# Kernel tuning notes

Hardware: AMD Instinct MI355X
Metric: run time of the kernel (lower is better)

## Reference

```python
import jax, jax.numpy as jnp
import numpy as np

# ---- problem constants (match init_kwargs / input_specs) ----
N = 10000        # atoms
E = 160000       # edges
G = 16           # graphs in batch
Z = 10           # num_elements
K = 64           # channels (count of 0e in hidden_irreps)
NB = 8           # num_bessel
SH = 9           # (max_ell+1)^2, max_ell=2
HID = 16         # MLP_irreps 16x0e
R_MAX = 5.0
AVG_NEI = 16.0
P = 5            # num_polynomial_cutoff
L_SLICES = ((0, 1, 0), (1, 4, 1), (4, 9, 2))  # (start, end, l) per irrep block


def _sph(u):
    # real spherical harmonics, 'component' normalization, lmax=2 -> 9 comps
    x, y, z = u[:, 0], u[:, 1], u[:, 2]
    s3, s15, s5 = 3.0 ** 0.5, 15.0 ** 0.5, 5.0 ** 0.5
    one = jnp.ones_like(x)
    return jnp.stack([one,
                      s3 * x, s3 * y, s3 * z,
                      s15 * x * y, s15 * y * z,
                      0.5 * s5 * (3.0 * z * z - 1.0),
                      s15 * x * z, 0.5 * s15 * (x * x - y * y)], axis=-1)


def _radial(r):
    # Bessel basis * polynomial cutoff (p=5)
    n = jnp.arange(1, NB + 1, dtype=r.dtype)
    bess = (2.0 / R_MAX) ** 0.5 * jnp.sin(n[None, :] * jnp.pi * r[:, None] / R_MAX) / r[:, None]
    xx = r / R_MAX
    f = (1.0 - 0.5 * (P + 1) * (P + 2) * xx ** P + P * (P + 2) * xx ** (P + 1)
         - 0.5 * P * (P + 1) * xx ** (P + 2)) * (xx < 1.0)
    return bess * f[:, None]


def _total_energy(positions, node_attrs, shifts, atomic_energies, W_embed, W_up,
                  R1, R2, R3, R4, W_out, W_sc, theta, W_mix, w_read0, Wr1, Wr2,
                  edge_index, batch):
    sender, receiver = edge_index[0], edge_index[1]
    vec = positions[receiver] - positions[sender] + shifts          # [E,3]
    r = jnp.sqrt(jnp.sum(vec * vec, axis=-1) + 1e-9)                # [E]
    u = vec / r[:, None]
    sh = _sph(u)                                                     # [E,9]
    edge_feats = _radial(r)                                          # [E,NB]

    node_e0 = node_attrs @ atomic_energies                           # [N]
    energies = jax.ops.segment_sum(node_e0, batch, num_segments=G)   # [G]

    feats = node_attrs @ W_embed                                     # [N,K] scalar feats
    for i in range(2):
        h = feats @ W_up[i]                                          # [N,K]
        xw = jax.nn.silu(edge_feats @ R1[i])
        xw = jax.nn.silu(xw @ R2[i])
        xw = jax.nn.silu(xw @ R3[i])
        rw = xw @ R4[i]                                              # [E,K] TP weights
        # channel-wise tensor product message + scatter to receiver
        m = rw[:, :, None] * h[sender][:, :, None] * sh[:, None, :]  # [E,K,9]
        A = jax.ops.segment_sum(m, receiver, num_segments=N) / AVG_NEI  # [N,K,9]
        A = jnp.concatenate([jnp.einsum('nkc,kj->njc', A[:, :, s:e], W_out[i, l])
                             for (s, e, l) in L_SLICES], axis=-1)    # per-l linear
        sc = jnp.einsum('nk,nz,zkj->nj', feats, node_attrs, W_sc[i])  # residual (0e)
        # symmetric-contraction product block (correlation=3), element-dependent
        a0 = A[:, :, 0]
        w = jnp.einsum('nz,pzk->pnk', node_attrs, theta[i])           # [3,N,K]
        B = (w[0] + w[1] * a0 + w[2] * a0 * a0)[:, :, None] * A      # [N,K,9]
        B = jnp.einsum('nkc,kj->njc', B, W_mix[i])
        B = B.at[:, :, 0].add(sc)
        feats = B[:, :, 0]                                            # invariant part
        if i == 0:
            node_e = feats @ w_read0                                  # linear readout
        else:
            node_e = jax.nn.silu(feats @ Wr1) @ Wr2                   # nonlinear readout
        energies = energies + jax.ops.segment_sum(node_e, batch, num_segments=G)
    return energies                                                   # [G]


def setup_inputs() -> dict:
    key = jax.random.key(0)
    ks = jax.random.split(key, 24)
    positions = jax.random.normal(ks[0], (N, 3), jnp.float32) * 1.5
    elems = jax.random.randint(ks[1], (N,), 0, Z)
    node_attrs = jax.nn.one_hot(elems, Z, dtype=jnp.float32)
    edge_index = jax.random.randint(ks[2], (2, E), 0, N)
    batch = jnp.sort(jax.random.randint(ks[3], (N,), 0, G))
    shifts = jnp.zeros((E, 3), jnp.float32)
    rn = lambda k, sh, s: jax.random.normal(k, sh, jnp.float32) * s
    return {
        'positions': positions, 'node_attrs': node_attrs, 'shifts': shifts,
        'atomic_energies': rn(ks[4], (Z,), 1.0),
        'W_embed': rn(ks[5], (Z, K), Z ** -0.5),
        'W_up': rn(ks[6], (2, K, K), K ** -0.5),
        'R1': rn(ks[7], (2, NB, 64), NB ** -0.5),
        'R2': rn(ks[8], (2, 64, 64), 64 ** -0.5),
        'R3': rn(ks[9], (2, 64, 64), 64 ** -0.5),
        'R4': rn(ks[10], (2, 64, K), 64 ** -0.5),
        'W_out': rn(ks[11], (2, 3, K, K), K ** -0.5),
        'W_sc': rn(ks[12], (2, Z, K, K), (Z * K) ** -0.5),
        'theta': rn(ks[13], (2, 3, Z, K), 0.1),
        'W_mix': rn(ks[14], (2, K, K), K ** -0.5),
        'w_read0': rn(ks[15], (K,), K ** -0.5),
        'Wr1': rn(ks[16], (K, HID), K ** -0.5),
        'Wr2': rn(ks[17], (HID,), HID ** -0.5),
        'edge_index': edge_index, 'batch': batch,
    }


def reference(positions, node_attrs, shifts, atomic_energies, W_embed, W_up,
              R1, R2, R3, R4, W_out, W_sc, theta, W_mix, w_read0, Wr1, Wr2,
              edge_index, batch):
    def energy(pos):
        return _total_energy(pos, node_attrs, shifts, atomic_energies, W_embed, W_up,
                             R1, R2, R3, R4, W_out, W_sc, theta, W_mix,
                             w_read0, Wr1, Wr2, edge_index, batch)
    total_energy, vjp_fn = jax.vjp(energy, positions)
    (g_pos,) = vjp_fn(jnp.ones((G,), positions.dtype))
    forces = -g_pos
    return total_energy, forces
```

## Files before the change

kernel.cpp:

```cpp
#include <hip/hip_runtime.h>
#include <math.h>

#define N_NODES 10000
#define N_EDGES 160000
#define G_SEG 16
#define ZDIM 10
#define KDIM 64
#define NBESS 8
#define HIDR 16
#define RMAXF 5.0f
#define AVG_NEI_F 16.0f
#define TBINS 256

__device__ __forceinline__ float siluf(float x){ float s = 1.0f/(1.0f+expf(-x)); return x*s; }
__device__ __forceinline__ float dsiluf(float x){ float s = 1.0f/(1.0f+expf(-x)); return s*(1.0f + x*(1.0f-s)); }

__device__ __forceinline__ float waveReduce(float v){
  for (int off = 32; off > 0; off >>= 1) v += __shfl_down(v, off);
  return v;
}

__device__ __forceinline__ void r_decode(float r, int& b, float& fr, float& wm){
  wm = (r >= 0.f) ? 1.f : 0.f;
  float tp = fmaxf(r, 0.f) * (TBINS / RMAXF);
  b = (int)tp; if (b > TBINS-1) b = TBINS-1;
  fr = tp - (float)b;
}

#define GATHER_NODE(NODE, PTR, PACK, IDXEXPR, LOADH, OUT) { \
  int beg_ = PTR[NODE]; int deg_ = PTR[(NODE)+1] - beg_; \
  float a0_=0.f,a1_=0.f,a2_=0.f,a3_=0.f; \
  for (int base_=0; base_<deg_; base_+=64){ \
    int m_ = min(64, deg_-base_); \
    float r_l = -1.f; int ix_l = 0; \
    if (lane < m_){ int4 pk = PACK[beg_+base_+lane]; r_l = __int_as_float(pk.x); ix_l = IDXEXPR; } \
    int mr_ = (m_ + 7) & ~7; \
    for (int i_=0; i_<mr_; i_+=8){ \
      float r0_=__shfl(r_l,i_),   r1_=__shfl(r_l,i_+1), r2_=__shfl(r_l,i_+2), r3_=__shfl(r_l,i_+3); \
      float r4_=__shfl(r_l,i_+4), r5_=__shfl(r_l,i_+5), r6_=__shfl(r_l,i_+6), r7_=__shfl(r_l,i_+7); \
      int s0_=__shfl(ix_l,i_),   s1_=__shfl(ix_l,i_+1), s2_=__shfl(ix_l,i_+2), s3_=__shfl(ix_l,i_+3); \
      int s4_=__shfl(ix_l,i_+4), s5_=__shfl(ix_l,i_+5), s6_=__shfl(ix_l,i_+6), s7_=__shfl(ix_l,i_+7); \
      int b0_,b1_,b2_,b3_,b4_,b5_,b6_,b7_; \
      float f0_,f1_,f2_,f3_,f4_,f5_,f6_,f7_, w0_,w1_,w2_,w3_,w4_,w5_,w6_,w7_; \
      r_decode(r0_,b0_,f0_,w0_); r_decode(r1_,b1_,f1_,w1_); r_decode(r2_,b2_,f2_,w2_); r_decode(r3_,b3_,f3_,w3_); \
      r_decode(r4_,b4_,f4_,w4_); r_decode(r5_,b5_,f5_,w5_); r_decode(r6_,b6_,f6_,w6_); r_decode(r7_,b7_,f7_,w7_); \
      float2 F0_=Ft2[b0_*KDIM+lane]; float h0_=LOADH(s0_); \
      float2 F1_=Ft2[b1_*KDIM+lane]; float h1_=LOADH(s1_); \
      float2 F2_=Ft2[b2_*KDIM+lane]; float h2_=LOADH(s2_); \
      float2 F3_=Ft2[b3_*KDIM+lane]; float h3_=LOADH(s3_); \
      float2 F4_=Ft2[b4_*KDIM+lane]; float h4_=LOADH(s4_); \
      float2 F5_=Ft2[b5_*KDIM+lane]; float h5_=LOADH(s5_); \
      float2 F6_=Ft2[b6_*KDIM+lane]; float h6_=LOADH(s6_); \
      float2 F7_=Ft2[b7_*KDIM+lane]; float h7_=LOADH(s7_); \
      a0_ += w0_*(F0_.x + f0_*(F0_.y-F0_.x))*h0_; a1_ += w1_*(F1_.x + f1_*(F1_.y-F1_.x))*h1_; \
      a2_ += w2_*(F2_.x + f2_*(F2_.y-F2_.x))*h2_; a3_ += w3_*(F3_.x + f3_*(F3_.y-F3_.x))*h3_; \
      a0_ += w4_*(F4_.x + f4_*(F4_.y-F4_.x))*h4_; a1_ += w5_*(F5_.x + f5_*(F5_.y-F5_.x))*h5_; \
      a2_ += w6_*(F6_.x + f6_*(F6_.y-F6_.x))*h6_; a3_ += w7_*(F7_.x + f7_*(F7_.y-F7_.x))*h7_; \
    } } \
  OUT = ((a0_+a1_)+(a2_+a3_)); }

#define COOPMV(INV, W, OUTV) { \
  lds_in[w][lane] = INV; \
  __syncthreads(); \
  { float p0_=0.f,p1_=0.f,p2_=0.f,p3__=0.f; \
    const float* Wb_ = (W) + (w*16)*KDIM + lane; \
    _Pragma("unroll") \
    for (int kk_=0; kk_<16; kk_++){ \
      float wrow_ = Wb_[kk_*KDIM]; \
      int k_ = w*16 + kk_; \
      p0_  += lds_in[0][k_]*wrow_; \
      p1_  += lds_in[1][k_]*wrow_; \
      p2_  += lds_in[2][k_]*wrow_; \
      p3__ += lds_in[3][k_]*wrow_; \
    } \
    lds_part[w][0][lane]=p0_; lds_part[w][1][lane]=p1_; \
    lds_part[w][2][lane]=p2_; lds_part[w][3][lane]=p3__; } \
  __syncthreads(); \
  OUTV = ((lds_part[0][w][lane]+lds_part[1][w][lane]) + \
          (lds_part[2][w][lane]+lds_part[3][w][lane])); }

#define MV4R(V, W, OUT) { \
  float x0_=0.f,x1_=0.f,x2_=0.f,x3_=0.f; \
  for (int k_=0;k_<KDIM;k_+=4){ \
    x0_ += __shfl(V,k_)  *W[k_*KDIM+lane]; \
    x1_ += __shfl(V,k_+1)*W[(k_+1)*KDIM+lane]; \
    x2_ += __shfl(V,k_+2)*W[(k_+2)*KDIM+lane]; \
    x3_ += __shfl(V,k_+3)*W[(k_+3)*KDIM+lane]; \
  } OUT = (x0_+x1_)+(x2_+x3_); }

#define LOADH_PLAIN(S) rows[(S)*KDIM + lane]
#define LOADH_G2(S)    gAr2c[(S)*KDIM + lane].x

__global__ __launch_bounds__(256) void k_setup(
    const float* We, const float* Wup, const float* Wsc,
    const float* Wout, const float* Wmix,
    const float* Wr1,
    const float* attrs, const float* aE,
    float* M0, float* Msc0,
    float* WoT0, float* WoT1, float* WmixT0, float* WupT1,
    float* P1, float* Qtab,
    int* z_buf, float* e_node){
  int blk = blockIdx.x, tid = threadIdx.x;
  const float* Wmix1 = Wmix + KDIM*KDIM;
  const float* Wsc1  = Wsc + ZDIM*KDIM*KDIM;
  if (blk < 5){
    int idx = blk*256 + tid;
    if (idx < 1280){
      int which = idx >= 640;
      int t = which ? idx - 640 : idx;
      int z = t >> 6, j = t & 63;
      float acc = 0.f;
      if (!which){
        #pragma unroll 8
        for (int k = 0; k < KDIM; k++) acc += We[z*KDIM + k] * Wup[k*KDIM + j];
        M0[z*KDIM + j] = acc;
      } else {
        #pragma unroll 8
        for (int k = 0; k < KDIM; k++) acc += We[z*KDIM + k] * Wsc[(z*KDIM + k)*KDIM + j];
        Msc0[z*KDIM + j] = acc;
      }
    }
  } else if (blk < 69){
    int t = (blk-5)*256 + tid;
    int arr = t >> 12;
    int rem = t & 4095;
    int j = rem >> 6, k = rem & 63;
    float v; float* dst;
    switch(arr){
      case 0: v = Wout[k*KDIM + j];                 dst = WoT0;   break;
      case 1: v = Wout[3*KDIM*KDIM + k*KDIM + j];   dst = WoT1;   break;
      case 2: v = Wmix[k*KDIM + j];                 dst = WmixT0; break;
      default:v = Wup[KDIM*KDIM + k*KDIM + j];      dst = WupT1;  break;
    }
    dst[rem] = v;
  } else if (blk < 73){
    int t = (blk-69)*256 + tid;
    int h = t >> 6, k = t & 63;
    float acc = 0.f;
    #pragma unroll 8
    for (int j = 0; j < KDIM; j++) acc += Wr1[j*HIDR + h] * Wmix1[k*KDIM + j];
    P1[h*KDIM + k] = acc;
  } else if (blk < 113){
    int t = (blk-73)*256 + tid;
    int z = t >> 10;
    int rem = t & 1023;
    int h = rem >> 6, k = rem & 63;
    float acc = 0.f;
    #pragma unroll 8
    for (int j = 0; j < KDIM; j++) acc += Wr1[j*HIDR + h] * Wsc1[(z*KDIM + k)*KDIM + j];
    Qtab[(z*HIDR + h)*KDIM + k] = acc;
  } else {
    int n = (blk-113)*256 + tid;
    if (n < N_NODES){
      int z = 0;
      for (int i = 1; i < ZDIM; i++) if (attrs[n*ZDIM+i] > 0.5f) z = i;
      z_buf[n] = z;
      e_node[n] = aE[z];
    }
  }
}

__global__ __launch_bounds__(256) void k_edge_setup(const float* pos, const float* shifts, const int* ei,
                                                    const int* z_buf,
                                                    float4* evec, int4* emeta,
                                                    int* cnt_r, int* cnt_s){
  int e = blockIdx.x*256 + threadIdx.x;
  int s = ei[e], rcv = ei[N_EDGES + e];
  float dx = pos[rcv*3+0] - pos[s*3+0] + shifts[e*3+0];
  float dy = pos[rcv*3+1] - pos[s*3+1] + shifts[e*3+1];
  float dz = pos[rcv*3+2] - pos[s*3+2] + shifts[e*3+2];
  float r = sqrtf(dx*dx + dy*dy + dz*dz + 1e-9f);
  evec[e] = make_float4(dx, dy, dz, r);
  emeta[e] = make_int4(__float_as_int(r), s, rcv, z_buf[s]);
  if (r < RMAXF){
    atomicAdd(&cnt_s[s], 1);
    atomicAdd(&cnt_r[rcv], 1);
  }
}

__global__ __launch_bounds__(1024) void k_scan(const int* cnt_r, int* ptr_r, int* cur_r,
                                               const int* cnt_s, int* ptr_s, int* cur_s){
  __shared__ int part[1024];
  int tid = threadIdx.x;
  const int* cnt = blockIdx.x ? cnt_s : cnt_r;
  int* ptr = blockIdx.x ? ptr_s : ptr_r;
  int* cur = blockIdx.x ? cur_s : cur_r;
  const int per = 10;
  int start = tid*per;
  int s = 0;
  for (int t = 0; t < per; t++){ int i = start + t; if (i < N_NODES) s += cnt[i]; }
  part[tid] = s; __syncthreads();
  for (int d = 1; d < 1024; d <<= 1){
    int v = (tid >= d) ? part[tid-d] : 0;
    __syncthreads();
    part[tid] += v;
    __syncthreads();
  }
  int run = part[tid] - s;
  for (int t = 0; t < per; t++){
    int i = start + t;
    if (i < N_NODES){ ptr[i] = run; cur[i] = run; run += cnt[i]; }
  }
  if (tid == 1023) ptr[N_NODES] = part[1023];
}

__global__ __launch_bounds__(256) void k_fill(const int4* emeta, int* cur_r, int* cur_s,
                                              int4* pr_pack, int4* ps_pack){
  int e = blockIdx.x*256 + threadIdx.x;
  int4 m = emeta[e];
  float r = __int_as_float(m.x);
  if (r >= RMAXF) return;
  int p = atomicAdd(&cur_s[m.y], 1);
  ps_pack[p] = make_int4(m.x, m.z, e, 0);
  int p2 = atomicAdd(&cur_r[m.z], 1);
  pr_pack[p2] = make_int4(m.x, m.y, m.w, e);
}

__global__ __launch_bounds__(64) void k_table(const float* R1g, const float* R2g,
                                              const float* R3g, const float* R4g,
                                              float2* Ft2_0, float2* Ft2_1, float* dF4f){
  int blk = blockIdx.x;
  int i = blk / (TBINS+1);
  int t = blk % (TBINS+1);
  int j = threadIdx.x;
  __shared__ float efs[NBESS], defs[NBESS];
  __shared__ float xs[KDIM], dxs[KDIM];
  if (j < NBESS){
    double r = (double)t * (double)RMAXF / (double)TBINS;
    double w = (double)(j+1) * M_PI / (double)RMAXF;
    double c = sqrt(2.0 / (double)RMAXF);
    double bess, dbess;
    if (r < 1e-12){ bess = c*w; dbess = 0.0; }
    else {
      double sw = sin(w*r), cw = cos(w*r);
      bess = c*sw/r;
      dbess = c*(w*cw*r - sw)/(r*r);
    }
    double xx = r / (double)RMAXF;
    double f = 0.0, df = 0.0;
    if (xx < 1.0){
      double x2 = xx*xx, x4 = x2*x2, x5 = x4*xx, x6 = x5*xx, x7 = x6*xx;
      f = 1.0 - 21.0*x5 + 35.0*x6 - 15.0*x7;
      df = (-105.0*x4 + 210.0*x5 - 105.0*x6) / (double)RMAXF;
    }
    efs[j]  = (float)(bess*f);
    defs[j] = (float)(dbess*f + bess*df);
  }
  __syncthreads();
  const float* R1 = R1g + i*NBESS*KDIM;
  const float* R2 = R2g + i*KDIM*KDIM;
  const float* R3 = R3g + i*KDIM*KDIM;
  const float* R4 = R4g + i*KDIM*KDIM;
  float z = 0.f, dz = 0.f;
  for (int b = 0; b < NBESS; b++){ float w = R1[b*KDIM+j]; z += efs[b]*w; dz += defs[b]*w; }
  float v = siluf(z), dv = dsiluf(z)*dz;
  xs[j] = v; dxs[j] = dv; __syncthreads();
  z = 0.f; dz = 0.f;
  for (int k = 0; k < KDIM; k++){ float w = R2[k*KDIM+j]; z += xs[k]*w; dz += dxs[k]*w; }
  v = siluf(z); dv = dsiluf(z)*dz; __syncthreads();
  xs[j] = v; dxs[j] = dv; __syncthreads();
  z = 0.f; dz = 0.f;
  for (int k = 0; k < KDIM; k++){ float w = R3[k*KDIM+j]; z += xs[k]*w; dz += dxs[k]*w; }
  v = siluf(z); dv = dsiluf(z)*dz; __syncthreads();
  xs[j] = v; dxs[j] = dv; __syncthreads();
  z = 0.f; dz = 0.f;
  for (int k = 0; k < KDIM; k++){ float w = R4[k*KDIM+j]; z += xs[k]*w; dz += dxs[k]*w; }
  float2* Ft  = i ? Ft2_1 : Ft2_0;
  Ft[t*KDIM+j].x = z;  if (t > 0) Ft[(t-1)*KDIM+j].y = z;
  dF4f[(t*KDIM+j)*4 + 2*i] = dz;
  if (t > 0) dF4f[((t-1)*KDIM+j)*4 + 2*i + 1] = dz;
}

__global__ __launch_bounds__(256) void k_layer0_fwd(
    const int* z_buf, const int* ptr_r, const int4* pr_pack,
    const float2* Ft2, const float* M0,
    const float* Wout0, const float* theta0, const float* Wmix0,
    const float* Msc0, const float* w_read0,
    const float* Wup1, const float* Wsc1,
    float* A0_out, float* h1, float* sc1, float* e_node){
  __shared__ float lds_in[4][KDIM];
  __shared__ float lds_part[4][4][KDIM];
  int tid = threadIdx.x;
  int w = tid >> 6, lane = tid & 63;
  int node = blockIdx.x*4 + w;
  int z = z_buf[node];
  const float* rows = M0;
  float acc;
  GATHER_NODE(node, ptr_r, pr_pack, pk.z, LOADH_PLAIN, acc)
  acc *= (1.0f/AVG_NEI_F);
  float a0;
  COOPMV(acc, Wout0, a0)
  A0_out[node*KDIM+lane] = a0;
  float t0 = theta0[(0*ZDIM+z)*KDIM+lane];
  float t1 = theta0[(1*ZDIM+z)*KDIM+lane];
  float t2 = theta0[(2*ZDIM+z)*KDIM+lane];
  float v = (t0 + t1*a0 + t2*a0*a0)*a0;
  float f;
  COOPMV(v, Wmix0, f)
  f += Msc0[z*KDIM+lane];
  float p = waveReduce(f * w_read0[lane]);
  if (lane == 0) e_node[node] += p;
  float h;
  COOPMV(f, Wup1, h)
  h1[node*KDIM+lane] = h;
  const float* Wz = Wsc1 + z*KDIM*KDIM;
  float s;
  MV4R(f, Wz, s)
  sc1[node*KDIM+lane] = s;
}

__global__ __launch_bounds__(256) void k_layer1_fwd_bwd(
    const int* z_buf, const int* ptr_r, const int4* pr_pack,
    const float2* Ft2, const float* h1,
    const float* Wout1, const float* theta1, const float* Wmix1,
    const float* sc1, const float* Wr1, const float* Wr2,
    const float* P1, const float* Qtab, const float* WoT1, const float* w_read0,
    float2* gAr2, float* gF1, float* e_node){
  __shared__ float lds_in[4][KDIM];
  __shared__ float lds_part[4][4][KDIM];
  int tid = threadIdx.x;
  int w = tid >> 6, lane = tid & 63;
  int node = blockIdx.x*4 + w;
  int z = z_buf[node];
  const float* rows = h1;
  float acc;
  GATHER_NODE(node, ptr_r, pr_pack, pk.y, LOADH_PLAIN, acc)
  acc *= (1.0f/AVG_NEI_F);
  float a0;
  COOPMV(acc, Wout1, a0)
  float t0 = theta1[(0*ZDIM+z)*KDIM+lane];
  float t1 = theta1[(1*ZDIM+z)*KDIM+lane];
  float t2 = theta1[(2*ZDIM+z)*KDIM+lane];
  float v = (t0 + t1*a0 + t2*a0*a0)*a0;
  float f;
  COOPMV(v, Wmix1, f)
  f += sc1[node*KDIM+lane];
  int hh = lane & 15;
  float tp0 = 0.f, tp1 = 0.f;
  for (int j = 0; j < KDIM; j += 2){
    tp0 += __shfl(f,j)  *Wr1[j*HIDR+hh];
    tp1 += __shfl(f,j+1)*Wr1[(j+1)*HIDR+hh];
  }
  float tpart = tp0 + tp1;
  float wr2 = Wr2[hh];
  float ne = waveReduce(siluf(tpart)*wr2);
  if (lane == 0) e_node[node] += 0.25f*ne;
  float coeff = dsiluf(tpart)*wr2;
  float gP0=0.f, gP1=0.f, gs0=0.f, gs1=0.f;
  const float* Qz = Qtab + z*HIDR*KDIM;
  #pragma unroll
  for (int h2 = 0; h2 < HIDR; h2 += 2){
    float c0 = __shfl(coeff, h2), c1 = __shfl(coeff, h2+1);
    gP0 += c0*P1[h2*KDIM+lane];
    gP1 += c1*P1[(h2+1)*KDIM+lane];
    gs0 += c0*Qz[h2*KDIM+lane];
    gs1 += c1*Qz[(h2+1)*KDIM+lane];
  }
  gF1[node*KDIM+lane] = w_read0[lane] + gs0 + gs1;
  float u = t0 + 2.f*t1*a0 + 3.f*t2*a0*a0;
  float vl = (gP0+gP1)*u;
  float gAr;
  COOPMV(vl, WoT1, gAr)
  gAr2[node*KDIM+lane].x = gAr * (1.0f/AVG_NEI_F);
}

__global__ __launch_bounds__(256) void k_energy(const float* e_node, const int* batch, float* out_e){
  __shared__ float part[G_SEG];
  int tid = threadIdx.x;
  if (tid < G_SEG) part[tid] = 0.f;
  __syncthreads();
  int n = blockIdx.x*256 + tid;
  if (n < N_NODES) atomicAdd(&part[batch[n]], e_node[n]);
  __syncthreads();
  if (tid < G_SEG) atomicAdd(&out_e[tid], part[tid]);
}

__global__ __launch_bounds__(256) void k_bwd_gH0(
    const int* z_buf, const int* ptr_s, const int4* ps_pack,
    const float2* Ft2, const float2* gAr2c, const float* WupT1, const float* gF1,
    const float* A00, const float* WmixT0, const float* WoT0, const float* theta0,
    float2* gAr2){
  __shared__ float lds_in[4][KDIM];
  __shared__ float lds_part[4][4][KDIM];
  int tid = threadIdx.x;
  int w = tid >> 6, lane = tid & 63;
  int node = blockIdx.x*4 + w;
  float ga;
  GATHER_NODE(node, ptr_s, ps_pack, pk.y, LOADH_G2, ga)
  float gfh;
  COOPMV(ga, WupT1, gfh)
  float gt = gF1[node*KDIM+lane] + gfh;
  float gP;
  COOPMV(gt, WmixT0, gP)
  int z = z_buf[node];
  float a = A00[node*KDIM+lane];
  float t0 = theta0[(0*ZDIM+z)*KDIM+lane];
  float t1 = theta0[(1*ZDIM+z)*KDIM+lane];
  float t2 = theta0[(2*ZDIM+z)*KDIM+lane];
  float u = t0 + 2.f*t1*a + 3.f*t2*a*a;
  float vl = gP*u;
  float gAr;
  COOPMV(vl, WoT0, gAr)
  gAr2[node*KDIM+lane].y = gAr * (1.0f/AVG_NEI_F);
}

__global__ __launch_bounds__(256) void k_gr(const int4* emeta, const float4* dF4,
                                            const float2* gAr2, const float* h1, const float* M0,
                                            float4* evec){
  int tid = threadIdx.x;
  int w = tid>>6, lane = tid&63;
  int e = blockIdx.x*4 + w;
  int4 m = emeta[e];
  float r = __int_as_float(m.x);
  if (r >= RMAXF) return;
  float tp = r * (TBINS / RMAXF);
  int b = (int)tp; if (b > TBINS-1) b = TBINS-1;
  float fr = tp - (float)b;
  float4 d4 = dF4[b*KDIM + lane];
  float2 g  = gAr2[m.z*KDIM + lane];
  float hv1 = h1[m.y*KDIM + lane];
  float hv0 = M0[m.w*KDIM + lane];
  float v = g.x*hv1*(d4.z + fr*(d4.w - d4.z)) + g.y*hv0*(d4.x + fr*(d4.y - d4.x));
  v = waveReduce(v);
  if (lane == 0) evec[e].w = v / r;
}

__global__ __launch_bounds__(256) void k_force(const int* ptr_r, const int4* pr_pack,
                                               const int* ptr_s, const int4* ps_pack,
                                               const float4* evec,
                                               float* out_f){
  int tid = threadIdx.x;
  int node = blockIdx.x*16 + (tid >> 4);
  int li = tid & 15;
  float fx=0.f, fy=0.f, fz=0.f;
  int beg = ptr_r[node], end = ptr_r[node+1];
  for (int idx = beg + li; idx < end; idx += 16){
    int e = pr_pack[idx].w;
    float4 ev = evec[e];
    fx -= ev.w*ev.x; fy -= ev.w*ev.y; fz -= ev.w*ev.z;
  }
  beg = ptr_s[node]; end = ptr_s[node+1];
  for (int idx = beg + li; idx < end; idx += 16){
    int e = ps_pack[idx].z;
    float4 ev = evec[e];
    fx += ev.w*ev.x; fy += ev.w*ev.y; fz += ev.w*ev.z;
  }
  #pragma unroll
  for (int off = 8; off > 0; off >>= 1){
    fx += __shfl_xor(fx, off);
    fy += __shfl_xor(fy, off);
    fz += __shfl_xor(fz, off);
  }
  if (li == 0){
    out_f[node*3+0] = fx; out_f[node*3+1] = fy; out_f[node*3+2] = fz;
  }
}

extern "C" void kernel_launch(void* const* d_in, const int* in_sizes, int n_in,
                              void* d_out, int out_size, void* d_ws, size_t ws_size,
                              hipStream_t stream){
  const float* pos    = (const float*)d_in[0];
  const float* attrs  = (const float*)d_in[1];
  const float* shifts = (const float*)d_in[2];
  const float* aE     = (const float*)d_in[3];
  const float* We     = (const float*)d_in[4];
  const float* Wup    = (const float*)d_in[5];
  const float* R1     = (const float*)d_in[6];
  const float* R2     = (const float*)d_in[7];
  const float* R3     = (const float*)d_in[8];
  const float* R4     = (const float*)d_in[9];
  const float* Wout   = (const float*)d_in[10];
  const float* Wsc    = (const float*)d_in[11];
  const float* theta  = (const float*)d_in[12];
  const float* Wmix   = (const float*)d_in[13];
  const float* w_read0= (const float*)d_in[14];
  const float* Wr1    = (const float*)d_in[15];
  const float* Wr2    = (const float*)d_in[16];
  const int*   ei     = (const int*)d_in[17];
  const int*   batch  = (const int*)d_in[18];

  char* base = (char*)d_ws;
  size_t off = 0;
  auto alloc = [&](size_t bytes)->void*{
    void* p = base + off;
    off = (off + bytes + 255) & ~(size_t)255;
    return p;
  };
  float4* evec   = (float4*)alloc(N_EDGES*sizeof(float4));
  int4*   emeta  = (int4*)alloc(N_EDGES*sizeof(int4));
  int4*   pr_pack= (int4*)alloc(N_EDGES*sizeof(int4));
  int4*   ps_pack= (int4*)alloc(N_EDGES*sizeof(int4));
  float*  e_node = (float*)alloc(N_NODES*sizeof(float));
  float*  h1     = (float*)alloc(N_NODES*KDIM*sizeof(float));
  float*  sc1    = (float*)alloc(N_NODES*KDIM*sizeof(float));
  float*  A00    = (float*)alloc(N_NODES*KDIM*sizeof(float));
  float*  gF1    = (float*)alloc(N_NODES*KDIM*sizeof(float));
  float2* gAr2   = (float2*)alloc(N_NODES*KDIM*sizeof(float2));
  float2* Ft2_0  = (float2*)alloc((TBINS+1)*KDIM*sizeof(float2));
  float2* Ft2_1  = (float2*)alloc((TBINS+1)*KDIM*sizeof(float2));
  float4* dF4    = (float4*)alloc((TBINS+1)*KDIM*sizeof(float4));
  float*  M0     = (float*)alloc(ZDIM*KDIM*sizeof(float));
  float*  Msc0   = (float*)alloc(ZDIM*KDIM*sizeof(float));
  float*  WoT0   = (float*)alloc(KDIM*KDIM*sizeof(float));
  float*  WoT1   = (float*)alloc(KDIM*KDIM*sizeof(float));
  float*  WmixT0 = (float*)alloc(KDIM*KDIM*sizeof(float));
  float*  WupT1  = (float*)alloc(KDIM*KDIM*sizeof(float));
  float*  P1     = (float*)alloc(HIDR*KDIM*sizeof(float));
  float*  Qtab   = (float*)alloc(ZDIM*HIDR*KDIM*sizeof(float));
  int* z_buf = (int*)alloc(N_NODES*sizeof(int));
  int* cnt_r = (int*)alloc(N_NODES*sizeof(int));
  int* cnt_s = (int*)alloc(N_NODES*sizeof(int));
  int* ptr_r = (int*)alloc((N_NODES+1)*sizeof(int));
  int* ptr_s = (int*)alloc((N_NODES+1)*sizeof(int));
  int* cur_r = (int*)alloc(N_NODES*sizeof(int));
  int* cur_s = (int*)alloc(N_NODES*sizeof(int));

  float* out_e = (float*)d_out;
  float* out_f = out_e + G_SEG;

  hipMemsetAsync(d_out, 0, (size_t)out_size*sizeof(float), stream);
  hipMemsetAsync(cnt_r, 0, N_NODES*sizeof(int), stream);
  hipMemsetAsync(cnt_s, 0, N_NODES*sizeof(int), stream);

  const int NB4 = N_NODES/4;
  const int EB  = N_EDGES/256;
  const int EB4 = N_EDGES/4;
  const int NBt = (N_NODES+255)/256;

  const float* Wup1 = Wup + KDIM*KDIM;
  const float* Wsc1 = Wsc + ZDIM*KDIM*KDIM;
  const float* Wout1 = Wout + 3*KDIM*KDIM;
  const float* theta1 = theta + 3*ZDIM*KDIM;
  const float* Wmix1 = Wmix + KDIM*KDIM;

  k_setup<<<153,256,0,stream>>>(We, Wup, Wsc, Wout, Wmix, Wr1, attrs, aE,
                                M0, Msc0, WoT0, WoT1, WmixT0, WupT1, P1, Qtab,
                                z_buf, e_node);
  k_table<<<2*(TBINS+1),64,0,stream>>>(R1, R2, R3, R4, Ft2_0, Ft2_1, (float*)dF4);
  k_edge_setup<<<EB,256,0,stream>>>(pos, shifts, ei, z_buf, evec, emeta, cnt_r, cnt_s);
  k_scan<<<2,1024,0,stream>>>(cnt_r, ptr_r, cur_r, cnt_s, ptr_s, cur_s);
  k_fill<<<EB,256,0,stream>>>(emeta, cur_r, cur_s, pr_pack, ps_pack);

  k_layer0_fwd<<<NB4,256,0,stream>>>(z_buf, ptr_r, pr_pack, Ft2_0, M0,
      Wout, theta, Wmix, Msc0, w_read0, Wup1, Wsc1,
      A00, h1, sc1, e_node);
  k_layer1_fwd_bwd<<<NB4,256,0,stream>>>(z_buf, ptr_r, pr_pack, Ft2_1, h1,
      Wout1, theta1, Wmix1, sc1, Wr1, Wr2,
      P1, Qtab, WoT1, w_read0,
      gAr2, gF1, e_node);
  k_energy<<<NBt,256,0,stream>>>(e_node, batch, out_e);

  k_bwd_gH0<<<NB4,256,0,stream>>>(z_buf, ptr_s, ps_pack, Ft2_1, gAr2, WupT1, gF1,
      A00, WmixT0, WoT0, theta, gAr2);
  k_gr<<<EB4,256,0,stream>>>(emeta, dF4, gAr2, h1, M0, evec);
  k_force<<<N_NODES/16,256,0,stream>>>(ptr_r, pr_pack, ptr_s, ps_pack, evec, out_f);
}
```

Before: 268.9 us.

## Fuse radial table build into setup kernel and use wave-shuffle scan

The separate radial-MLP table kernel is folded into k_setup as extra blocks, with one wave per table row and activations passed between lanes by shuffles rather than LDS and barriers. k_scan replaces its 1024-step LDS Hillis-Steele scan, which used two barriers per step, with a wave-level shuffle scan plus a 16-entry cross-wave pass. Together these remove one kernel launch and most block-wide syncs in two small serial stages. The cost is that every lane now computes the double-precision Bessel terms, including lanes beyond the 8 basis functions whose values are never read.

```diff
diff --git a/kernel.cpp b/kernel.cpp
--- a/kernel.cpp
+++ b/kernel.cpp
@@ -91,14 +91,20 @@
 #define LOADH_PLAIN(S) rows[(S)*KDIM + lane]
 #define LOADH_G2(S)    gAr2c[(S)*KDIM + lane].x
 
+#define NTABW 514
+#define SETUP_BASE 153
+#define NSETUP (SETUP_BASE + (NTABW+3)/4)
+
 __global__ __launch_bounds__(256) void k_setup(
     const float* We, const float* Wup, const float* Wsc,
     const float* Wout, const float* Wmix,
     const float* Wr1,
     const float* attrs, const float* aE,
+    const float* R1g, const float* R2g, const float* R3g, const float* R4g,
     float* M0, float* Msc0,
     float* WoT0, float* WoT1, float* WmixT0, float* WupT1,
     float* P1, float* Qtab,
+    float2* Ft2_0, float2* Ft2_1, float* dF4f,
     int* z_buf, float* e_node){
   int blk = blockIdx.x, tid = threadIdx.x;
   const float* Wmix1 = Wmix + KDIM*KDIM;
@@ -149,7 +155,7 @@
     #pragma unroll 8
     for (int j = 0; j < KDIM; j++) acc += Wr1[j*HIDR + h] * Wsc1[(z*KDIM + k)*KDIM + j];
     Qtab[(z*HIDR + h)*KDIM + k] = acc;
-  } else {
+  } else if (blk < SETUP_BASE){
     int n = (blk-113)*256 + tid;
     if (n < N_NODES){
       int z = 0;
@@ -157,6 +163,70 @@
       z_buf[n] = z;
       e_node[n] = aE[z];
     }
+  } else {
+    int w = tid >> 6, j = tid & 63;
+    int wave_id = (blk - SETUP_BASE)*4 + w;
+    if (wave_id >= NTABW) return;
+    int i = wave_id / (TBINS+1);
+    int t = wave_id % (TBINS+1);
+    float efv = 0.f, defv = 0.f;
+    {
+      double r = (double)t * (double)RMAXF / (double)TBINS;
+      double wfr = (double)(j+1) * M_PI / (double)RMAXF;
+      double c = sqrt(2.0 / (double)RMAXF);
+      double bess, dbess;
+      if (r < 1e-12){ bess = c*wfr; dbess = 0.0; }
+      else {
+        double sw = sin(wfr*r), cw = cos(wfr*r);
+        bess = c*sw/r;
+        dbess = c*(wfr*cw*r - sw)/(r*r);
+      }
+      double xx = r / (double)RMAXF;
+      double f = 0.0, df = 0.0;
+      if (xx < 1.0){
+        double x2 = xx*xx, x4 = x2*x2, x5 = x4*xx, x6 = x5*xx, x7 = x6*xx;
+        f = 1.0 - 21.0*x5 + 35.0*x6 - 15.0*x7;
+        df = (-105.0*x4 + 210.0*x5 - 105.0*x6) / (double)RMAXF;
+      }
+      efv  = (float)(bess*f);
+      defv = (float)(dbess*f + bess*df);
+    }
+    const float* R1 = R1g + i*NBESS*KDIM;
+    const float* R2 = R2g + i*KDIM*KDIM;
+    const float* R3 = R3g + i*KDIM*KDIM;
+    const float* R4 = R4g + i*KDIM*KDIM;
+    float z = 0.f, dz = 0.f;
+    #pragma unroll
+    for (int b = 0; b < NBESS; b++){
+      float ef = __shfl(efv, b), def = __shfl(defv, b);
+      float wv = R1[b*KDIM+j];
+      z += ef*wv; dz += def*wv;
+    }
+    float v = siluf(z), dv = dsiluf(z)*dz;
+    z = 0.f; dz = 0.f;
+    for (int k = 0; k < KDIM; k++){
+      float xv = __shfl(v, k), dxv = __shfl(dv, k);
+      float wv = R2[k*KDIM+j];
+      z += xv*wv; dz += dxv*wv;
+    }
+    float v2 = siluf(z), dv2 = dsiluf(z)*dz;
+    z = 0.f; dz = 0.f;
+    for (int k = 0; k < KDIM; k++){
+      float xv = __shfl(v2, k), dxv = __shfl(dv2, k);
+      float wv = R3[k*KDIM+j];
+      z += xv*wv; dz += dxv*wv;
+    }
+    float v3 = siluf(z), dv3 = dsiluf(z)*dz;
+    z = 0.f; dz = 0.f;
+    for (int k = 0; k < KDIM; k++){
+      float xv = __shfl(v3, k), dxv = __shfl(dv3, k);
+      float wv = R4[k*KDIM+j];
+      z += xv*wv; dz += dxv*wv;
+    }
+    float2* Ft = i ? Ft2_1 : Ft2_0;
+    Ft[t*KDIM+j].x = z;  if (t > 0) Ft[(t-1)*KDIM+j].y = z;
+    dF4f[(t*KDIM+j)*4 + 2*i] = dz;
+    if (t > 0) dF4f[((t-1)*KDIM+j)*4 + 2*i + 1] = dz;
   }
 }
 
@@ -180,28 +250,51 @@
 
 __global__ __launch_bounds__(1024) void k_scan(const int* cnt_r, int* ptr_r, int* cur_r,
                                                const int* cnt_s, int* ptr_s, int* cur_s){
-  __shared__ int part[1024];
-  int tid = threadIdx.x;
+  __shared__ float dummy;
+  __shared__ int wtot[16];
+  __shared__ int woff[16];
+  (void)dummy;
+  int tid = threadIdx.x;
+  int w = tid >> 6, lane = tid & 63;
   const int* cnt = blockIdx.x ? cnt_s : cnt_r;
   int* ptr = blockIdx.x ? ptr_s : ptr_r;
   int* cur = blockIdx.x ? cur_s : cur_r;
   const int per = 10;
   int start = tid*per;
-  int s = 0;
-  for (int t = 0; t < per; t++){ int i = start + t; if (i < N_NODES) s += cnt[i]; }
-  part[tid] = s; __syncthreads();
-  for (int d = 1; d < 1024; d <<= 1){
-    int v = (tid >= d) ? part[tid-d] : 0;
-    __syncthreads();
-    part[tid] += v;
-    __syncthreads();
-  }
-  int run = part[tid] - s;
+  int csum = 0;
+  int cl[per];
+  #pragma unroll
   for (int t = 0; t < per; t++){
     int i = start + t;
-    if (i < N_NODES){ ptr[i] = run; cur[i] = run; run += cnt[i]; }
-  }
-  if (tid == 1023) ptr[N_NODES] = part[1023];
+    int c = (i < N_NODES) ? cnt[i] : 0;
+    cl[t] = c; csum += c;
+  }
+  int v = csum;
+  #pragma unroll
+  for (int off = 1; off < 64; off <<= 1){
+    int u = __shfl_up(v, off);
+    if (lane >= off) v += u;
+  }
+  if (lane == 63) wtot[w] = v;
+  __syncthreads();
+  if (w == 0 && lane < 16){
+    int t = wtot[lane];
+    int sv = t;
+    #pragma unroll
+    for (int off = 1; off < 16; off <<= 1){
+      int u = __shfl_up(sv, off);
+      if (lane >= off) sv += u;
+    }
+    woff[lane] = sv - t;
+    if (lane == 15) ptr[N_NODES] = sv;
+  }
+  __syncthreads();
+  int run = woff[w] + v - csum;
+  #pragma unroll
+  for (int t = 0; t < per; t++){
+    int i = start + t;
+    if (i < N_NODES){ ptr[i] = run; cur[i] = run; run += cl[t]; }
+  }
 }
 
 __global__ __launch_bounds__(256) void k_fill(const int4* emeta, int* cur_r, int* cur_s,
@@ -214,61 +307,6 @@
   ps_pack[p] = make_int4(m.x, m.z, e, 0);
   int p2 = atomicAdd(&cur_r[m.z], 1);
   pr_pack[p2] = make_int4(m.x, m.y, m.w, e);
-}
-
-__global__ __launch_bounds__(64) void k_table(const float* R1g, const float* R2g,
-                                              const float* R3g, const float* R4g,
-                                              float2* Ft2_0, float2* Ft2_1, float* dF4f){
-  int blk = blockIdx.x;
-  int i = blk / (TBINS+1);
-  int t = blk % (TBINS+1);
-  int j = threadIdx.x;
-  __shared__ float efs[NBESS], defs[NBESS];
-  __shared__ float xs[KDIM], dxs[KDIM];
-  if (j < NBESS){
-    double r = (double)t * (double)RMAXF / (double)TBINS;
-    double w = (double)(j+1) * M_PI / (double)RMAXF;
-    double c = sqrt(2.0 / (double)RMAXF);
-    double bess, dbess;
-    if (r < 1e-12){ bess = c*w; dbess = 0.0; }
-    else {
-      double sw = sin(w*r), cw = cos(w*r);
-      bess = c*sw/r;
-      dbess = c*(w*cw*r - sw)/(r*r);
-    }
-    double xx = r / (double)RMAXF;
-    double f = 0.0, df = 0.0;
-    if (xx < 1.0){
-      double x2 = xx*xx, x4 = x2*x2, x5 = x4*xx, x6 = x5*xx, x7 = x6*xx;
-      f = 1.0 - 21.0*x5 + 35.0*x6 - 15.0*x7;
-      df = (-105.0*x4 + 210.0*x5 - 105.0*x6) / (double)RMAXF;
-    }
-    efs[j]  = (float)(bess*f);
-    defs[j] = (float)(dbess*f + bess*df);
-  }
-  __syncthreads();
-  const float* R1 = R1g + i*NBESS*KDIM;
-  const float* R2 = R2g + i*KDIM*KDIM;
-  const float* R3 = R3g + i*KDIM*KDIM;
-  const float* R4 = R4g + i*KDIM*KDIM;
-  float z = 0.f, dz = 0.f;
-  for (int b = 0; b < NBESS; b++){ float w = R1[b*KDIM+j]; z += efs[b]*w; dz += defs[b]*w; }
-  float v = siluf(z), dv = dsiluf(z)*dz;
-  xs[j] = v; dxs[j] = dv; __syncthreads();
-  z = 0.f; dz = 0.f;
-  for (int k = 0; k < KDIM; k++){ float w = R2[k*KDIM+j]; z += xs[k]*w; dz += dxs[k]*w; }
-  v = siluf(z); dv = dsiluf(z)*dz; __syncthreads();
-  xs[j] = v; dxs[j] = dv; __syncthreads();
-  z = 0.f; dz = 0.f;
-  for (int k = 0; k < KDIM; k++){ float w = R3[k*KDIM+j]; z += xs[k]*w; dz += dxs[k]*w; }
-  v = siluf(z); dv = dsiluf(z)*dz; __syncthreads();
-  xs[j] = v; dxs[j] = dv; __syncthreads();
-  z = 0.f; dz = 0.f;
-  for (int k = 0; k < KDIM; k++){ float w = R4[k*KDIM+j]; z += xs[k]*w; dz += dxs[k]*w; }
-  float2* Ft  = i ? Ft2_1 : Ft2_0;
-  Ft[t*KDIM+j].x = z;  if (t > 0) Ft[(t-1)*KDIM+j].y = z;
-  dF4f[(t*KDIM+j)*4 + 2*i] = dz;
-  if (t > 0) dF4f[((t-1)*KDIM+j)*4 + 2*i + 1] = dz;
 }
 
 __global__ __launch_bounds__(256) void k_layer0_fwd(
@@ -533,10 +571,11 @@
   const float* theta1 = theta + 3*ZDIM*KDIM;
   const float* Wmix1 = Wmix + KDIM*KDIM;
 
-  k_setup<<<153,256,0,stream>>>(We, Wup, Wsc, Wout, Wmix, Wr1, attrs, aE,
-                                M0, Msc0, WoT0, WoT1, WmixT0, WupT1, P1, Qtab,
-                                z_buf, e_node);
-  k_table<<<2*(TBINS+1),64,0,stream>>>(R1, R2, R3, R4, Ft2_0, Ft2_1, (float*)dF4);
+  k_setup<<<NSETUP,256,0,stream>>>(We, Wup, Wsc, Wout, Wmix, Wr1, attrs, aE,
+                                   R1, R2, R3, R4,
+                                   M0, Msc0, WoT0, WoT1, WmixT0, WupT1, P1, Qtab,
+                                   Ft2_0, Ft2_1, (float*)dF4,
+                                   z_buf, e_node);
   k_edge_setup<<<EB,256,0,stream>>>(pos, shifts, ei, z_buf, evec, emeta, cnt_r, cnt_s);
   k_scan<<<2,1024,0,stream>>>(cnt_r, ptr_r, cur_r, cnt_s, ptr_s, cur_s);
   k_fill<<<EB,256,0,stream>>>(emeta, cur_r, cur_s, pr_pack, ps_pack);
```

New measurement: 265.4 us. About the same (-1.3%).
